# Optimization experiments

Measured on AMD Instinct MI355X. Metric: run time of the kernel, lower is better.

The kernel has to match this reference:

```python
import jax, jax.numpy as jnp
import numpy as np

B = 8192
D_IN = 512
D_HID = 256
D_OUT = 128
EPS_STD = 1e-5
EPS_NORM = 1e-12


def _embed(x, W1, b1, W2, b2):
    # head: Linear -> ReLU -> Linear
    h = jax.nn.relu(x @ W1 + b1)          # (b, 256)
    y = h @ W2 + b2                        # (b, 128)
    # white(): per-feature batch whitening (center + unit std, unbiased like torch.std)
    mu = jnp.mean(y, axis=0, keepdims=True)
    sd = jnp.std(y, axis=0, keepdims=True, ddof=1) + EPS_STD
    y = (y - mu) / sd
    # F.normalize(p=2, dim=1)
    n = jnp.maximum(jnp.linalg.norm(y, axis=1, keepdims=True), EPS_NORM)
    return y / n


def _pair_loss(v1, v2):
    b = v1.shape[0]
    cat = jnp.concatenate([v1, v2], axis=0)            # (2b, d)
    inner = v1 @ cat.T                                  # (b, 2b) == broadcasted (v1*cat).sum(2)
    mask = jnp.concatenate(
        [1.0 - jnp.eye(b, dtype=inner.dtype), jnp.ones((b, b), dtype=inner.dtype)], axis=1)
    logits = inner * mask                               # zero out self-similarity logits
    logp = jax.nn.log_softmax(logits, axis=1)
    tgt = jnp.arange(b, 2 * b)                          # positive = matching row in v2 block
    return -jnp.take_along_axis(logp, tgt[:, None], axis=1).mean()


def setup_inputs() -> dict:
    key = jax.random.key(0)
    ks = jax.random.split(key, 16)
    def lin_init(k, fin, fout):
        bound = 1.0 / np.sqrt(fin)
        kw, kb = jax.random.split(k)
        W = jax.random.uniform(kw, (fin, fout), jnp.float32, -bound, bound)
        b = jax.random.uniform(kb, (fout,), jnp.float32, -bound, bound)
        return W, b
    inp = {
        'x_B': jax.random.normal(ks[0], (B, D_IN), jnp.float32),
        'x_E': jax.random.normal(ks[1], (B, D_IN), jnp.float32),
        'x_F': jax.random.normal(ks[2], (B, D_IN), jnp.float32),
    }
    for i, m in enumerate('BEF'):
        W1, b1 = lin_init(ks[3 + 2 * i], D_IN, D_HID)
        W2, b2 = lin_init(ks[4 + 2 * i], D_HID, D_OUT)
        inp[f'W1_{m}'] = W1; inp[f'b1_{m}'] = b1
        inp[f'W2_{m}'] = W2; inp[f'b2_{m}'] = b2
    return inp


def reference(x_B, x_E, x_F,
              W1_B, b1_B, W2_B, b2_B,
              W1_E, b1_E, W2_E, b2_E,
              W1_F, b1_F, W2_F, b2_F):
    zB = _embed(x_B, W1_B, b1_B, W2_B, b2_B)
    zE = _embed(x_E, W1_E, b1_E, W2_E, b2_E)
    zF = _embed(x_F, W1_F, b1_F, W2_F, b2_F)
    pairs = [(zB, zE), (zB, zF), (zE, zF)]  # itertools.combinations order
    loss = sum(_pair_loss(v1, v2) for v1, v2 in pairs) / len(pairs)
    return loss
```

## Files before the change

kernel.cpp:

```cpp
#include <hip/hip_runtime.h>
#include <hip/hip_bf16.h>
#include <math.h>

#define NROWS 8192
#define DIN   512
#define DHID  256
#define DOUT  128
#define LOG2E 1.4426950408889634f

typedef unsigned short ushort_t;
typedef __attribute__((ext_vector_type(8))) short bf16x8;
typedef __attribute__((ext_vector_type(4))) float f32x4;

#if defined(__has_builtin)
#  if __has_builtin(__builtin_amdgcn_exp2f)
#    define FAST_EXP2(x) __builtin_amdgcn_exp2f(x)
#  else
#    define FAST_EXP2(x) exp2f(x)
#  endif
#else
#  define FAST_EXP2(x) exp2f(x)
#endif

__device__ __forceinline__ short f2bf(float x) {
  __hip_bfloat16 h = __float2bfloat16(x);
  return *(short*)&h;
}

__device__ __forceinline__ bf16x8 cvt8(float4 lo, float4 hi) {
  bf16x8 r;
  r[0] = f2bf(lo.x); r[1] = f2bf(lo.y); r[2] = f2bf(lo.z); r[3] = f2bf(lo.w);
  r[4] = f2bf(hi.x); r[5] = f2bf(hi.y); r[6] = f2bf(hi.z); r[7] = f2bf(hi.w);
  return r;
}

__device__ __forceinline__ void dma16(const void* g, void* l) {
  __builtin_amdgcn_global_load_lds(
      (const __attribute__((address_space(1))) unsigned int*)g,
      (__attribute__((address_space(3))) unsigned int*)l, 16, 0, 0);
}

__global__ __launch_bounds__(256) void prep_w_kernel(
    const float* __restrict__ W1_0, const float* __restrict__ W1_1,
    const float* __restrict__ W1_2,
    const float* __restrict__ W2_0, const float* __restrict__ W2_1,
    const float* __restrict__ W2_2,
    ushort_t* __restrict__ w1t3, ushort_t* __restrict__ w2t3)
{
  const int z = blockIdx.y;
  const float* W1 = z == 0 ? W1_0 : (z == 1 ? W1_1 : W1_2);
  const float* W2 = z == 0 ? W2_0 : (z == 1 ? W2_1 : W2_2);
  int idx = blockIdx.x * 256 + threadIdx.x;
  if (idx < DHID * DIN) {
    int n = idx >> 9, k = idx & (DIN - 1);
    w1t3[(size_t)z * DHID * DIN + idx] = f2bf(W1[(size_t)k * DHID + n]);
  } else {
    int j = idx - DHID * DIN;
    int n = j >> 8, k = j & (DHID - 1);
    w2t3[(size_t)z * DOUT * DHID + j] = f2bf(W2[(size_t)k * DOUT + n]);
  }
}

#define MLP_BUF 20480
__global__ __launch_bounds__(256, 3) void mlp_kernel(
    const float* __restrict__ x0, const float* __restrict__ x1,
    const float* __restrict__ x2,
    const ushort_t* __restrict__ w1t3,
    const float* __restrict__ b1_0, const float* __restrict__ b1_1,
    const float* __restrict__ b1_2,
    const ushort_t* __restrict__ w2t3,
    const float* __restrict__ b2_0, const float* __restrict__ b2_1,
    const float* __restrict__ b2_2,
    float* __restrict__ y3,
    float* __restrict__ colsum, float* __restrict__ colsumsq)
{
  const int z = blockIdx.y;
  const float* X  = z == 0 ? x0 : (z == 1 ? x1 : x2);
  const float* B1 = z == 0 ? b1_0 : (z == 1 ? b1_1 : b1_2);
  const float* B2 = z == 0 ? b2_0 : (z == 1 ? b2_1 : b2_2);
  const ushort_t* W1t = w1t3 + (size_t)z * DHID * DIN;
  const ushort_t* W2t = w2t3 + (size_t)z * DOUT * DHID;
  float* Y    = y3 + (size_t)z * NROWS * DOUT;
  float* csum = colsum + z * DOUT;
  float* csq  = colsumsq + z * DOUT;

  __shared__ __align__(16) char lds[2 * MLP_BUF];
  ushort_t* hs = (ushort_t*)lds;

  const int tid = threadIdx.x, lane = tid & 63, wave = tid >> 6;
  const int quad = lane >> 4, l16 = lane & 15;
  const int m0 = blockIdx.x * 32;

  const char* w1b = (const char*)W1t;
  const char* wsrc[4];
#pragma unroll
  for (int jj = 0; jj < 4; jj++)
    wsrc[jj] = w1b + (size_t)(16 * (wave * 4 + jj) + l16) * 1024 +
               (lane >> 4) * 16;
  const int row8 = lane >> 3, slot = lane & 7;
  const int gseg = (slot + row8) & 7;
  const char* xsrc = (const char*)X +
      (size_t)(m0 + 8 * wave + row8) * 2048 + gseg * 16;

  f32x4 acc1[2][4] = {};
#pragma unroll
  for (int jj = 0; jj < 4; jj++)
    dma16(wsrc[jj], lds + (wave * 4 + jj) * 1024);
  dma16(xsrc, lds + 16384 + wave * 1024);
  __syncthreads();

  for (int c = 0; c < 16; c++) {
    const int buf = c & 1;
    if (c + 1 < 16) {
      char* dst = lds + (buf ^ 1) * MLP_BUF;
#pragma unroll
      for (int jj = 0; jj < 4; jj++)
        dma16(wsrc[jj] + (c + 1) * 64, dst + (wave * 4 + jj) * 1024);
      dma16(xsrc + (c + 1) * 128, dst + 16384 + wave * 1024);
    }
    const char* wb = lds + buf * MLP_BUF;
    const char* xb = wb + 16384;
    bf16x8 a[2];
#pragma unroll
    for (int mt = 0; mt < 2; mt++) {
      const int r = mt * 16 + l16, r7 = r & 7;
      const int s0 = (2 * quad - r7) & 7, s1 = (2 * quad + 1 - r7) & 7;
      float4 v0 = *(const float4*)(xb + r * 128 + s0 * 16);
      float4 v1 = *(const float4*)(xb + r * 128 + s1 * 16);
      a[mt] = cvt8(v0, v1);
    }
    bf16x8 b[4];
#pragma unroll
    for (int ct = 0; ct < 4; ct++)
      b[ct] = *(const bf16x8*)(wb + (wave * 4 + ct) * 1024 + quad * 256 +
                               l16 * 16);
#pragma unroll
    for (int mt = 0; mt < 2; mt++)
#pragma unroll
      for (int ct = 0; ct < 4; ct++)
        acc1[mt][ct] = __builtin_amdgcn_mfma_f32_16x16x32_bf16(
            a[mt], b[ct], acc1[mt][ct], 0, 0, 0);
    __syncthreads();
  }

  bf16x8 b2f[2][8];
#pragma unroll
  for (int ct = 0; ct < 2; ct++)
#pragma unroll
    for (int kk = 0; kk < 8; kk++)
      b2f[ct][kk] = *(const bf16x8*)(W2t +
          (size_t)(wave * 32 + ct * 16 + l16) * DHID + kk * 32 + quad * 8);

#pragma unroll
  for (int ct = 0; ct < 4; ct++) {
    float bb = B1[wave * 64 + ct * 16 + l16];
#pragma unroll
    for (int mt = 0; mt < 2; mt++)
#pragma unroll
      for (int reg = 0; reg < 4; reg++) {
        float v = fmaxf(acc1[mt][ct][reg] + bb, 0.0f);
        hs[(mt * 16 + quad * 4 + reg) * 264 + wave * 64 + ct * 16 + l16] =
            (ushort_t)f2bf(v);
      }
  }
  __syncthreads();

  f32x4 acc2[2][2] = {};
#pragma unroll
  for (int kk = 0; kk < 8; kk++) {
    bf16x8 a2[2];
#pragma unroll
    for (int mt = 0; mt < 2; mt++)
      a2[mt] = *(const bf16x8*)(hs + (mt * 16 + l16) * 264 + kk * 32 +
                                quad * 8);
#pragma unroll
    for (int mt = 0; mt < 2; mt++)
#pragma unroll
      for (int ct = 0; ct < 2; ct++)
        acc2[mt][ct] = __builtin_amdgcn_mfma_f32_16x16x32_bf16(
            a2[mt], b2f[ct][kk], acc2[mt][ct], 0, 0, 0);
  }

#pragma unroll
  for (int ct = 0; ct < 2; ct++) {
    const int colo = wave * 32 + ct * 16 + l16;
    float bb = B2[colo];
    float cs = 0.0f, cq = 0.0f;
#pragma unroll
    for (int mt = 0; mt < 2; mt++)
#pragma unroll
      for (int reg = 0; reg < 4; reg++) {
        float v = acc2[mt][ct][reg] + bb;
        Y[(size_t)(m0 + mt * 16 + quad * 4 + reg) * DOUT + colo] = v;
        cs += v; cq += v * v;
      }
    cs += __shfl_xor(cs, 16, 64); cs += __shfl_xor(cs, 32, 64);
    cq += __shfl_xor(cq, 16, 64); cq += __shfl_xor(cq, 32, 64);
    if (lane < 16) {
      atomicAdd(&csum[colo], cs);
      atomicAdd(&csq[colo], cq);
    }
  }
}

__global__ void stats_kernel(const float* __restrict__ colsum,
                             const float* __restrict__ colsumsq,
                             float* __restrict__ meanv, float* __restrict__ invsd)
{
  int i = threadIdx.x;
  if (i < 3 * DOUT) {
    float mu  = colsum[i] / (float)NROWS;
    float var = (colsumsq[i] - (float)NROWS * mu * mu) / (float)(NROWS - 1);
    float sd  = sqrtf(fmaxf(var, 0.0f)) + 1e-5f;
    meanv[i] = mu;
    invsd[i] = 1.0f / sd;
  }
}

__global__ __launch_bounds__(128) void whiten_kernel(
    const float* __restrict__ y3,
    const float* __restrict__ meanv, const float* __restrict__ invsd,
    ushort_t* __restrict__ zB, ushort_t* __restrict__ zE,
    ushort_t* __restrict__ zF,
    ushort_t* __restrict__ zBs, ushort_t* __restrict__ zEs,
    float* __restrict__ pos)
{
  int row = blockIdx.x, t = threadIdx.x;
  size_t off = (size_t)row * DOUT + t;
  const size_t hs = (size_t)NROWS * DOUT;
  float vB = (y3[off]          - meanv[t])            * invsd[t];
  float vE = (y3[off + hs]     - meanv[DOUT + t])     * invsd[DOUT + t];
  float vF = (y3[off + 2 * hs] - meanv[2 * DOUT + t]) * invsd[2 * DOUT + t];

  __shared__ float red[6], red2[6];
  float nB = vB * vB, nE = vE * vE, nF = vF * vF;
#pragma unroll
  for (int o = 32; o > 0; o >>= 1) {
    nB += __shfl_down(nB, o, 64);
    nE += __shfl_down(nE, o, 64);
    nF += __shfl_down(nF, o, 64);
  }
  int lane = t & 63, wv = t >> 6;
  if (lane == 0) { red[wv * 3] = nB; red[wv * 3 + 1] = nE; red[wv * 3 + 2] = nF; }
  __syncthreads();
  float iB = 1.0f / fmaxf(sqrtf(red[0] + red[3]), 1e-12f);
  float iE = 1.0f / fmaxf(sqrtf(red[1] + red[4]), 1e-12f);
  float iF = 1.0f / fmaxf(sqrtf(red[2] + red[5]), 1e-12f);
  float zb = vB * iB, ze = vE * iE, zf = vF * iF;

  zB[off]  = (ushort_t)f2bf(zb);
  zE[off]  = (ushort_t)f2bf(ze);
  zF[off]  = (ushort_t)f2bf(zf);
  zBs[off] = (ushort_t)f2bf(zb * LOG2E);
  zEs[off] = (ushort_t)f2bf(ze * LOG2E);

  float pBE = zb * ze, pBF = zb * zf, pEF = ze * zf;
#pragma unroll
  for (int o = 32; o > 0; o >>= 1) {
    pBE += __shfl_down(pBE, o, 64);
    pBF += __shfl_down(pBF, o, 64);
    pEF += __shfl_down(pEF, o, 64);
  }
  if (lane == 0) { red2[wv * 3] = pBE; red2[wv * 3 + 1] = pBF; red2[wv * 3 + 2] = pEF; }
  __syncthreads();
  if (t == 0) {
    pos[row]             = red2[0] + red2[3];
    pos[NROWS + row]     = red2[1] + red2[4];
    pos[2 * NROWS + row] = red2[2] + red2[5];
  }
}

#define G_CH  32
#define G_NCH 32
__global__ __launch_bounds__(256, 3) void gram_kernel(
    const ushort_t* __restrict__ zB, const ushort_t* __restrict__ zE,
    const ushort_t* __restrict__ zF,
    const ushort_t* __restrict__ zBs, const ushort_t* __restrict__ zEs,
    float* __restrict__ rowsum)
{
  const ushort_t *U, *V;
  float* rs;
  switch (blockIdx.z) {
    case 0:  U = zBs; V = zB; rs = rowsum;             break;
    case 1:  U = zEs; V = zE; rs = rowsum + NROWS;     break;
    case 2:  U = zBs; V = zE; rs = rowsum + 2 * NROWS; break;
    case 3:  U = zBs; V = zF; rs = rowsum + 3 * NROWS; break;
    default: U = zEs; V = zF; rs = rowsum + 4 * NROWS; break;
  }

  const int tid = threadIdx.x, lane = tid & 63, wave = tid >> 6;
  const int quad = lane >> 4, l16 = lane & 15;
  const int m0 = blockIdx.x * 256 + wave * 64;
  const int col0 = blockIdx.y * (G_CH * G_NCH);

  __shared__ __align__(16) ushort_t sbuf[2][4096];

  const ushort_t* ua = U + (size_t)(m0 + l16) * DOUT + quad * 8;
  bf16x8 a[4][4];
#pragma unroll
  for (int rt = 0; rt < 4; rt++)
#pragma unroll
    for (int ki = 0; ki < 4; ki++)
      a[rt][ki] = *(const bf16x8*)(ua + rt * 16 * DOUT + ki * 32);

  const char* Vb = (const char*)V;
  const int r_ = lane & 31, hi_ = lane >> 5;
  const int s0 = 4 * wave + hi_, s1 = 4 * wave + 2 + hi_;
  const char* g0 = Vb + (size_t)(col0 + r_) * 256 + (s0 >> 2) * 64 + (s0 & 3) * 16;
  const char* g1 = Vb + (size_t)(col0 + r_) * 256 + (s1 >> 2) * 64 + (s1 & 3) * 16;

  float rsum[4][4] = {};
  const f32x4 zero = {0.0f, 0.0f, 0.0f, 0.0f};

  dma16(g0, &sbuf[0][(2 * wave) * 512]);
  dma16(g1, &sbuf[0][(2 * wave + 1) * 512]);
  __syncthreads();

  for (int c = 0; c < G_NCH; c++) {
    const int buf = c & 1;
    if (c + 1 < G_NCH) {
      const size_t go = (size_t)(c + 1) * 8192;
      dma16(g0 + go, &sbuf[buf ^ 1][(2 * wave) * 512]);
      dma16(g1 + go, &sbuf[buf ^ 1][(2 * wave + 1) * 512]);
    }
    const char* sb = (const char*)&sbuf[buf][0];
    bf16x8 b[4][2];
#pragma unroll
    for (int ki = 0; ki < 4; ki++)
#pragma unroll
      for (int ct = 0; ct < 2; ct++)
        b[ki][ct] = *(const bf16x8*)(sb + (ki * 4 + quad) * 512 +
                                     (ct * 16 + l16) * 16);
    f32x4 acc[4][2];
#pragma unroll
    for (int ki = 0; ki < 4; ki++)
#pragma unroll
      for (int rt = 0; rt < 4; rt++)
#pragma unroll
        for (int ct = 0; ct < 2; ct++)
          acc[rt][ct] = __builtin_amdgcn_mfma_f32_16x16x32_bf16(
              a[rt][ki], b[ki][ct], ki == 0 ? zero : acc[rt][ct], 0, 0, 0);
#pragma unroll
    for (int rt = 0; rt < 4; rt++)
#pragma unroll
      for (int reg = 0; reg < 4; reg++)
        rsum[rt][reg] += FAST_EXP2(acc[rt][0][reg]) + FAST_EXP2(acc[rt][1][reg]);
    __syncthreads();
  }

#pragma unroll
  for (int rt = 0; rt < 4; rt++)
#pragma unroll
    for (int reg = 0; reg < 4; reg++) {
      float s = rsum[rt][reg];
      s += __shfl_xor(s, 1, 64);
      s += __shfl_xor(s, 2, 64);
      s += __shfl_xor(s, 4, 64);
      s += __shfl_xor(s, 8, 64);
      if (l16 == 0)
        atomicAdd(&rs[m0 + rt * 16 + quad * 4 + reg], s);
    }
}

__global__ __launch_bounds__(1024) void loss_kernel(
    const float* __restrict__ rowsum, const float* __restrict__ pos,
    float* __restrict__ out)
{
  const float* sB  = rowsum;
  const float* sE  = rowsum + NROWS;
  const float* cBE = rowsum + 2 * NROWS;
  const float* cBF = rowsum + 3 * NROWS;
  const float* cEF = rowsum + 4 * NROWS;
  const float* pBE = pos;
  const float* pBF = pos + NROWS;
  const float* pEF = pos + 2 * NROWS;

  const float corr = 1.0f - expf(1.0f);
  float local = 0.0f;
  for (int i = threadIdx.x; i < NROWS; i += 1024) {
    float selB = sB[i] + corr;
    float selE = sE[i] + corr;
    local += __logf(selB + cBE[i]) - pBE[i];
    local += __logf(selB + cBF[i]) - pBF[i];
    local += __logf(selE + cEF[i]) - pEF[i];
  }
  __shared__ float red[16];
#pragma unroll
  for (int o = 32; o > 0; o >>= 1) local += __shfl_down(local, o, 64);
  int lane = threadIdx.x & 63, wv = threadIdx.x >> 6;
  if (lane == 0) red[wv] = local;
  __syncthreads();
  if (threadIdx.x == 0) {
    float t = 0.0f;
#pragma unroll
    for (int w = 0; w < 16; w++) t += red[w];
    out[0] = t / (3.0f * (float)NROWS);
  }
}

extern "C" void kernel_launch(void* const* d_in, const int* in_sizes, int n_in,
                              void* d_out, int out_size, void* d_ws, size_t ws_size,
                              hipStream_t stream)
{
  const float* xs[3] = {(const float*)d_in[0], (const float*)d_in[1], (const float*)d_in[2]};
  const float* W1[3] = {(const float*)d_in[3], (const float*)d_in[7],  (const float*)d_in[11]};
  const float* b1[3] = {(const float*)d_in[4], (const float*)d_in[8],  (const float*)d_in[12]};
  const float* W2[3] = {(const float*)d_in[5], (const float*)d_in[9],  (const float*)d_in[13]};
  const float* b2[3] = {(const float*)d_in[6], (const float*)d_in[10], (const float*)d_in[14]};

  float* ws = (float*)d_ws;
  float* colsum   = ws;
  float* colsumsq = ws + 384;
  float* rowsum   = ws + 768;
  float* meanv    = ws + 41728;
  float* invsd    = ws + 42112;
  float* pos      = ws + 42496;
  ushort_t* w1t3 = (ushort_t*)(ws + 67072);
  ushort_t* w2t3 = (ushort_t*)(ws + 263680);
  float*    y3   = ws + 312832;
  ushort_t* zB   = (ushort_t*)(ws + 3458560);
  ushort_t* zE   = zB  + (size_t)NROWS * DOUT;
  ushort_t* zF   = zE  + (size_t)NROWS * DOUT;
  ushort_t* zBs  = zF  + (size_t)NROWS * DOUT;
  ushort_t* zEs  = zBs + (size_t)NROWS * DOUT;

  hipMemsetAsync(ws, 0, 41728 * sizeof(float), stream);

  prep_w_kernel<<<dim3(640, 3), 256, 0, stream>>>(
      W1[0], W1[1], W1[2], W2[0], W2[1], W2[2], w1t3, w2t3);
  mlp_kernel<<<dim3(256, 3), 256, 0, stream>>>(
      xs[0], xs[1], xs[2], w1t3, b1[0], b1[1], b1[2],
      w2t3, b2[0], b2[1], b2[2], y3, colsum, colsumsq);
  stats_kernel<<<1, 3 * DOUT, 0, stream>>>(colsum, colsumsq, meanv, invsd);
  whiten_kernel<<<NROWS, 128, 0, stream>>>(
      y3, meanv, invsd, zB, zE, zF, zBs, zEs, pos);
  gram_kernel<<<dim3(32, 8, 5), 256, 0, stream>>>(zB, zE, zF, zBs, zEs, rowsum);
  loss_kernel<<<1, 1024, 0, stream>>>(rowsum, pos, (float*)d_out);
}
```

Measured before the change: 237.0 us.

## Fold memset and stats into other kernels, wave-per-row whiten, larger gram chunks

```diff
diff --git a/kernel.cpp b/kernel.cpp
--- a/kernel.cpp
+++ b/kernel.cpp
@@ -45,9 +45,12 @@
     const float* __restrict__ W1_2,
     const float* __restrict__ W2_0, const float* __restrict__ W2_1,
     const float* __restrict__ W2_2,
-    ushort_t* __restrict__ w1t3, ushort_t* __restrict__ w2t3)
+    ushort_t* __restrict__ w1t3, ushort_t* __restrict__ w2t3,
+    float* __restrict__ zero_region)
 {
   const int z = blockIdx.y;
+  if (z == 0 && blockIdx.x < 163)
+    zero_region[blockIdx.x * 256 + threadIdx.x] = 0.0f;
   const float* W1 = z == 0 ? W1_0 : (z == 1 ? W1_1 : W1_2);
   const float* W2 = z == 0 ? W2_0 : (z == 1 ? W2_1 : W2_2);
   int idx = blockIdx.x * 256 + threadIdx.x;
@@ -203,75 +206,85 @@
   }
 }
 
-__global__ void stats_kernel(const float* __restrict__ colsum,
-                             const float* __restrict__ colsumsq,
-                             float* __restrict__ meanv, float* __restrict__ invsd)
-{
-  int i = threadIdx.x;
-  if (i < 3 * DOUT) {
-    float mu  = colsum[i] / (float)NROWS;
-    float var = (colsumsq[i] - (float)NROWS * mu * mu) / (float)(NROWS - 1);
-    float sd  = sqrtf(fmaxf(var, 0.0f)) + 1e-5f;
-    meanv[i] = mu;
-    invsd[i] = 1.0f / sd;
-  }
-}
-
-__global__ __launch_bounds__(128) void whiten_kernel(
+__global__ __launch_bounds__(256) void whiten_kernel(
     const float* __restrict__ y3,
-    const float* __restrict__ meanv, const float* __restrict__ invsd,
+    const float* __restrict__ colsum, const float* __restrict__ colsumsq,
     ushort_t* __restrict__ zB, ushort_t* __restrict__ zE,
     ushort_t* __restrict__ zF,
     ushort_t* __restrict__ zBs, ushort_t* __restrict__ zEs,
     float* __restrict__ pos)
 {
-  int row = blockIdx.x, t = threadIdx.x;
-  size_t off = (size_t)row * DOUT + t;
-  const size_t hs = (size_t)NROWS * DOUT;
-  float vB = (y3[off]          - meanv[t])            * invsd[t];
-  float vE = (y3[off + hs]     - meanv[DOUT + t])     * invsd[DOUT + t];
-  float vF = (y3[off + 2 * hs] - meanv[2 * DOUT + t]) * invsd[2 * DOUT + t];
-
-  __shared__ float red[6], red2[6];
-  float nB = vB * vB, nE = vE * vE, nF = vF * vF;
-#pragma unroll
-  for (int o = 32; o > 0; o >>= 1) {
-    nB += __shfl_down(nB, o, 64);
-    nE += __shfl_down(nE, o, 64);
-    nF += __shfl_down(nF, o, 64);
-  }
-  int lane = t & 63, wv = t >> 6;
-  if (lane == 0) { red[wv * 3] = nB; red[wv * 3 + 1] = nE; red[wv * 3 + 2] = nF; }
-  __syncthreads();
-  float iB = 1.0f / fmaxf(sqrtf(red[0] + red[3]), 1e-12f);
-  float iE = 1.0f / fmaxf(sqrtf(red[1] + red[4]), 1e-12f);
-  float iF = 1.0f / fmaxf(sqrtf(red[2] + red[5]), 1e-12f);
-  float zb = vB * iB, ze = vE * iE, zf = vF * iF;
-
-  zB[off]  = (ushort_t)f2bf(zb);
-  zE[off]  = (ushort_t)f2bf(ze);
-  zF[off]  = (ushort_t)f2bf(zf);
-  zBs[off] = (ushort_t)f2bf(zb * LOG2E);
-  zEs[off] = (ushort_t)f2bf(ze * LOG2E);
-
-  float pBE = zb * ze, pBF = zb * zf, pEF = ze * zf;
-#pragma unroll
-  for (int o = 32; o > 0; o >>= 1) {
-    pBE += __shfl_down(pBE, o, 64);
-    pBF += __shfl_down(pBF, o, 64);
-    pEF += __shfl_down(pEF, o, 64);
-  }
-  if (lane == 0) { red2[wv * 3] = pBE; red2[wv * 3 + 1] = pBF; red2[wv * 3 + 2] = pEF; }
-  __syncthreads();
-  if (t == 0) {
-    pos[row]             = red2[0] + red2[3];
-    pos[NROWS + row]     = red2[1] + red2[4];
-    pos[2 * NROWS + row] = red2[2] + red2[5];
-  }
-}
-
-#define G_CH  32
-#define G_NCH 32
+  const int tid = threadIdx.x, lane = tid & 63, wave = tid >> 6;
+  const int row = blockIdx.x * 4 + wave;
+  const size_t base = (size_t)row * DOUT;
+  const size_t hsz = (size_t)NROWS * DOUT;
+  const int c0 = lane, c1 = lane + 64;
+
+  float mu[3][2], isd[3][2];
+#pragma unroll
+  for (int h = 0; h < 3; h++) {
+#pragma unroll
+    for (int cc = 0; cc < 2; cc++) {
+      const int idx = h * DOUT + (cc ? c1 : c0);
+      float m = colsum[idx] * (1.0f / NROWS);
+      float var = (colsumsq[idx] - (float)NROWS * m * m) *
+                  (1.0f / (NROWS - 1));
+      mu[h][cc] = m;
+      isd[h][cc] = 1.0f / (sqrtf(fmaxf(var, 0.0f)) + 1e-5f);
+    }
+  }
+
+  float vB0 = (y3[base + c0]           - mu[0][0]) * isd[0][0];
+  float vB1 = (y3[base + c1]           - mu[0][1]) * isd[0][1];
+  float vE0 = (y3[base + hsz + c0]     - mu[1][0]) * isd[1][0];
+  float vE1 = (y3[base + hsz + c1]     - mu[1][1]) * isd[1][1];
+  float vF0 = (y3[base + 2 * hsz + c0] - mu[2][0]) * isd[2][0];
+  float vF1 = (y3[base + 2 * hsz + c1] - mu[2][1]) * isd[2][1];
+
+  float nB = vB0 * vB0 + vB1 * vB1;
+  float nE = vE0 * vE0 + vE1 * vE1;
+  float nF = vF0 * vF0 + vF1 * vF1;
+#pragma unroll
+  for (int o = 1; o < 64; o <<= 1) {
+    nB += __shfl_xor(nB, o, 64);
+    nE += __shfl_xor(nE, o, 64);
+    nF += __shfl_xor(nF, o, 64);
+  }
+  float iB = 1.0f / fmaxf(sqrtf(nB), 1e-12f);
+  float iE = 1.0f / fmaxf(sqrtf(nE), 1e-12f);
+  float iF = 1.0f / fmaxf(sqrtf(nF), 1e-12f);
+  float zb0 = vB0 * iB, zb1 = vB1 * iB;
+  float ze0 = vE0 * iE, ze1 = vE1 * iE;
+  float zf0 = vF0 * iF, zf1 = vF1 * iF;
+
+  zB[base + c0]  = (ushort_t)f2bf(zb0);
+  zB[base + c1]  = (ushort_t)f2bf(zb1);
+  zE[base + c0]  = (ushort_t)f2bf(ze0);
+  zE[base + c1]  = (ushort_t)f2bf(ze1);
+  zF[base + c0]  = (ushort_t)f2bf(zf0);
+  zF[base + c1]  = (ushort_t)f2bf(zf1);
+  zBs[base + c0] = (ushort_t)f2bf(zb0 * LOG2E);
+  zBs[base + c1] = (ushort_t)f2bf(zb1 * LOG2E);
+  zEs[base + c0] = (ushort_t)f2bf(ze0 * LOG2E);
+  zEs[base + c1] = (ushort_t)f2bf(ze1 * LOG2E);
+
+  float pBE = zb0 * ze0 + zb1 * ze1;
+  float pBF = zb0 * zf0 + zb1 * zf1;
+  float pEF = ze0 * zf0 + ze1 * zf1;
+#pragma unroll
+  for (int o = 1; o < 64; o <<= 1) {
+    pBE += __shfl_xor(pBE, o, 64);
+    pBF += __shfl_xor(pBF, o, 64);
+    pEF += __shfl_xor(pEF, o, 64);
+  }
+  if (lane == 0) {
+    pos[row]             = pBE;
+    pos[NROWS + row]     = pBF;
+    pos[2 * NROWS + row] = pEF;
+  }
+}
+
+#define G_NCH 16
 __global__ __launch_bounds__(256, 3) void gram_kernel(
     const ushort_t* __restrict__ zB, const ushort_t* __restrict__ zE,
     const ushort_t* __restrict__ zF,
@@ -291,9 +304,9 @@
   const int tid = threadIdx.x, lane = tid & 63, wave = tid >> 6;
   const int quad = lane >> 4, l16 = lane & 15;
   const int m0 = blockIdx.x * 256 + wave * 64;
-  const int col0 = blockIdx.y * (G_CH * G_NCH);
-
-  __shared__ __align__(16) ushort_t sbuf[2][4096];
+  const int col0 = blockIdx.y * (64 * G_NCH);
+
+  __shared__ __align__(16) ushort_t sbuf[2][8192];
 
   const ushort_t* ua = U + (size_t)(m0 + l16) * DOUT + quad * 8;
   bf16x8 a[4][4];
@@ -306,45 +319,53 @@
   const char* Vb = (const char*)V;
   const int r_ = lane & 31, hi_ = lane >> 5;
   const int s0 = 4 * wave + hi_, s1 = 4 * wave + 2 + hi_;
-  const char* g0 = Vb + (size_t)(col0 + r_) * 256 + (s0 >> 2) * 64 + (s0 & 3) * 16;
-  const char* g1 = Vb + (size_t)(col0 + r_) * 256 + (s1 >> 2) * 64 + (s1 & 3) * 16;
+  const char* g0 = Vb + (size_t)(col0 + r_) * 256 + s0 * 16;
+  const char* g1 = Vb + (size_t)(col0 + r_) * 256 + s1 * 16;
 
   float rsum[4][4] = {};
   const f32x4 zero = {0.0f, 0.0f, 0.0f, 0.0f};
 
   dma16(g0, &sbuf[0][(2 * wave) * 512]);
   dma16(g1, &sbuf[0][(2 * wave + 1) * 512]);
+  dma16(g0 + 8192, &sbuf[0][4096 + (2 * wave) * 512]);
+  dma16(g1 + 8192, &sbuf[0][4096 + (2 * wave + 1) * 512]);
   __syncthreads();
 
   for (int c = 0; c < G_NCH; c++) {
     const int buf = c & 1;
     if (c + 1 < G_NCH) {
-      const size_t go = (size_t)(c + 1) * 8192;
+      const size_t go = (size_t)(c + 1) * 16384;
       dma16(g0 + go, &sbuf[buf ^ 1][(2 * wave) * 512]);
       dma16(g1 + go, &sbuf[buf ^ 1][(2 * wave + 1) * 512]);
-    }
-    const char* sb = (const char*)&sbuf[buf][0];
-    bf16x8 b[4][2];
-#pragma unroll
-    for (int ki = 0; ki < 4; ki++)
-#pragma unroll
-      for (int ct = 0; ct < 2; ct++)
-        b[ki][ct] = *(const bf16x8*)(sb + (ki * 4 + quad) * 512 +
-                                     (ct * 16 + l16) * 16);
-    f32x4 acc[4][2];
-#pragma unroll
-    for (int ki = 0; ki < 4; ki++)
+      dma16(g0 + go + 8192, &sbuf[buf ^ 1][4096 + (2 * wave) * 512]);
+      dma16(g1 + go + 8192, &sbuf[buf ^ 1][4096 + (2 * wave + 1) * 512]);
+    }
+#pragma unroll
+    for (int h = 0; h < 2; h++) {
+      const char* sb = (const char*)&sbuf[buf][h * 4096];
+      bf16x8 b[4][2];
+#pragma unroll
+      for (int ki = 0; ki < 4; ki++)
+#pragma unroll
+        for (int ct = 0; ct < 2; ct++)
+          b[ki][ct] = *(const bf16x8*)(sb + (ki * 4 + quad) * 512 +
+                                       (ct * 16 + l16) * 16);
+      f32x4 acc[4][2];
+#pragma unroll
+      for (int ki = 0; ki < 4; ki++)
+#pragma unroll
+        for (int rt = 0; rt < 4; rt++)
+#pragma unroll
+          for (int ct = 0; ct < 2; ct++)
+            acc[rt][ct] = __builtin_amdgcn_mfma_f32_16x16x32_bf16(
+                a[rt][ki], b[ki][ct], ki == 0 ? zero : acc[rt][ct], 0, 0, 0);
 #pragma unroll
       for (int rt = 0; rt < 4; rt++)
 #pragma unroll
-        for (int ct = 0; ct < 2; ct++)
-          acc[rt][ct] = __builtin_amdgcn_mfma_f32_16x16x32_bf16(
-              a[rt][ki], b[ki][ct], ki == 0 ? zero : acc[rt][ct], 0, 0, 0);
-#pragma unroll
-    for (int rt = 0; rt < 4; rt++)
-#pragma unroll
-      for (int reg = 0; reg < 4; reg++)
-        rsum[rt][reg] += FAST_EXP2(acc[rt][0][reg]) + FAST_EXP2(acc[rt][1][reg]);
+        for (int reg = 0; reg < 4; reg++)
+          rsum[rt][reg] += FAST_EXP2(acc[rt][0][reg]) +
+                           FAST_EXP2(acc[rt][1][reg]);
+    }
     __syncthreads();
   }
 
@@ -412,8 +433,6 @@
   float* colsum   = ws;
   float* colsumsq = ws + 384;
   float* rowsum   = ws + 768;
-  float* meanv    = ws + 41728;
-  float* invsd    = ws + 42112;
   float* pos      = ws + 42496;
   ushort_t* w1t3 = (ushort_t*)(ws + 67072);
   ushort_t* w2t3 = (ushort_t*)(ws + 263680);
@@ -424,16 +443,13 @@
   ushort_t* zBs  = zF  + (size_t)NROWS * DOUT;
   ushort_t* zEs  = zBs + (size_t)NROWS * DOUT;
 
-  hipMemsetAsync(ws, 0, 41728 * sizeof(float), stream);
-
   prep_w_kernel<<<dim3(640, 3), 256, 0, stream>>>(
-      W1[0], W1[1], W1[2], W2[0], W2[1], W2[2], w1t3, w2t3);
+      W1[0], W1[1], W1[2], W2[0], W2[1], W2[2], w1t3, w2t3, ws);
   mlp_kernel<<<dim3(256, 3), 256, 0, stream>>>(
       xs[0], xs[1], xs[2], w1t3, b1[0], b1[1], b1[2],
       w2t3, b2[0], b2[1], b2[2], y3, colsum, colsumsq);
-  stats_kernel<<<1, 3 * DOUT, 0, stream>>>(colsum, colsumsq, meanv, invsd);
-  whiten_kernel<<<NROWS, 128, 0, stream>>>(
-      y3, meanv, invsd, zB, zE, zF, zBs, zEs, pos);
+  whiten_kernel<<<2048, 256, 0, stream>>>(
+      y3, colsum, colsumsq, zB, zE, zF, zBs, zEs, pos);
   gram_kernel<<<dim3(32, 8, 5), 256, 0, stream>>>(zB, zE, zF, zBs, zEs, rowsum);
   loss_kernel<<<1, 1024, 0, stream>>>(rowsum, pos, (float*)d_out);
 }
```

Result: slower. 266.9 us (+12.6%).
